# Kernel tuning notes

Hardware: AMD Instinct MI355X
Metric: run time of the kernel (lower is better)

## Reference

```python
import jax, jax.numpy as jnp
import numpy as np

B, T, L = 256, 512, 64


def setup_inputs() -> dict:
    key = jax.random.key(0)
    k1, k2, k3 = jax.random.split(key, 3)
    labels = jax.random.randint(k1, (B, T), 0, L)
    y_true = jax.nn.one_hot(labels, L, dtype=jnp.float32)  # [B,T,L] one-hot gold path
    y_pred = jax.random.normal(k2, (B, T, L), dtype=jnp.float32)  # emission scores
    # glorot_uniform init for trans [L,L]
    limit = np.sqrt(6.0 / (L + L)).astype(np.float32)
    trans = jax.random.uniform(k3, (L, L), dtype=jnp.float32, minval=-limit, maxval=limit)
    return {"y_true": y_true, "y_pred": y_pred, "trans": trans}


def reference(y_true, y_pred, trans):
    # ignore_last_label=False -> mask is None, all labels used.
    # Forward-algorithm log-partition via scan over time.
    init = y_pred[:, 0]  # [B,L]

    def step(state, emit_t):
        # state: [B,L] log-alpha; emit_t: [B,L]
        new = jax.nn.logsumexp(state[:, :, None] + trans[None, :, :], axis=1) + emit_t
        return new, None

    emits = jnp.swapaxes(y_pred[:, 1:], 0, 1)  # [T-1,B,L]
    last, _ = jax.lax.scan(step, init, emits)
    log_norm = jax.nn.logsumexp(last, axis=1, keepdims=True)  # [B,1]

    # path_score: per-label emission score + transition score along gold path
    point_score = jnp.sum(y_pred * y_true, axis=(1, 2))[:, None]  # [B,1]
    trans_score = jnp.einsum('bti,btj,ij->b', y_true[:, :-1], y_true[:, 1:], trans)[:, None]
    return -(point_score + trans_score - log_norm)  # [B,1] loss per example
```

## Files before the change

kernel.cpp:

```cpp
#include <hip/hip_runtime.h>
#include <hip/hip_bf16.h>
#include <cstdint>
#include <cstddef>


constexpr int Bc = 256, Tc = 512, Lc = 64;
#define LOG64F 4.1588830833596715f

typedef __attribute__((ext_vector_type(8))) short v8s;
typedef __attribute__((ext_vector_type(4))) float v4f;
typedef __attribute__((ext_vector_type(4))) unsigned int v4u;

__device__ __forceinline__ float lane_bcast(float v, int lane) {
    return __uint_as_float(__builtin_amdgcn_readlane(__float_as_uint(v), lane));
}
__device__ __forceinline__ int lane_bcast_i(int v, int lane) {
    return __builtin_amdgcn_readlane(v, lane);
}
__device__ __forceinline__ unsigned pk2(float x, float y) {
    const unsigned ux = __float_as_uint(x) + 0x8000u;
    const unsigned uy = __float_as_uint(y) + 0x8000u;
    return __builtin_amdgcn_perm(uy, ux, 0x07060302u);
}
__device__ __forceinline__ unsigned pk2t(float x, float y) {
    return __builtin_amdgcn_perm(__float_as_uint(y), __float_as_uint(x), 0x07060302u);
}
__device__ __forceinline__ v8s as_v8s(v4u u) {
    v8s r; __builtin_memcpy(&r, &u, 16); return r;
}
__device__ __forceinline__ unsigned short bf16b(float x) {
    return (unsigned short)((__float_as_uint(x) + 0x8000u) >> 16);
}

template<int CH>
__global__ __launch_bounds__(256, 2) void crf_pass1(
    const float* __restrict__ y_true,
    const float* __restrict__ y_pred,
    const float* __restrict__ trans,
    unsigned short* __restrict__ wsm,
    float* __restrict__ wss)
{
    constexpr int S = Tc / CH;
    const int tid = threadIdx.x, lane = tid & 63, wv = tid >> 6;
    const int w = blockIdx.x * 4 + wv;
    const int batch = w / CH;
    const int chunk = w % CH;
    const int q = lane >> 4, m16 = lane & 15;
    const int rsub = q, csub = m16;

    __shared__ alignas(16) unsigned char smem_raw[32768];
    float* strans = (float*)smem_raw;
    __shared__ alignas(16) float fbuf[4][4][Lc];

    {
        const v4f* t4 = (const v4f*)trans;
        #pragma unroll
        for (int k = 0; k < 4; ++k) {
            v4f v = t4[k * 256 + tid];
            *(v4f*)&strans[(k * 256 + tid) * 4] = v;
        }
    }
    __syncthreads();

    v8s Areg[4][2];
    #pragma unroll
    for (int I = 0; I < 4; ++I) {
        #pragma unroll
        for (int K = 0; K < 2; ++K) {
            float e[8];
            #pragma unroll
            for (int jj = 0; jj < 8; ++jj) {
                const int sig = (jj & 3) + 4 * q + 16 * (jj >> 2) + 32 * K;
                e[jj] = __expf(strans[sig * Lc + 16 * I + m16]);
            }
            v4u u;
            u.x = pk2(e[0], e[1]); u.y = pk2(e[2], e[3]);
            u.z = pk2(e[4], e[5]); u.w = pk2(e[6], e[7]);
            Areg[I][K] = as_v8s(u);
        }
    }

    const float* yp = y_pred + (size_t)batch * Tc * Lc;
    const float* yt = y_true + (size_t)batch * Tc * Lc;
    const v4f* yp4 = (const v4f*)yp;
    const v4f* yt4 = (const v4f*)yt;

    const int base = chunk * S;
    const int r0 = base + 1;
    float psum = 0.0f, tsum = 0.0f, c = 0.0f;
    int lbl_carry;
    {
        const float bt = yt[base * Lc + lane];
        lbl_carry = (int)__builtin_ctzll(__ballot(bt > 0.5f));
    }

    auto ld4 = [&](const v4f* p, int baseRow) -> v4f {
        int r = baseRow + rsub; r = (r < Tc - 1) ? r : (Tc - 1);
        return p[r * 16 + csub];
    };

    const v4f z4 = {0.f, 0.f, 0.f, 0.f};
    v4f cyp = ld4(yp4, r0), nyp = ld4(yp4, r0 + 4);
    v4f cyt = ld4(yt4, r0), nyt = ld4(yt4, r0 + 4);

    {
        const float k0 = lane_bcast(cyp.x, 0)  + LOG64F;
        const float k1 = lane_bcast(cyp.x, 16) + LOG64F;
        const float k2 = lane_bcast(cyp.x, 32) + LOG64F;
        const float k3 = lane_bcast(cyp.x, 48) + LOG64F;
        c += ((k0 + k1) + (k2 + k3));
        const float kk = (rsub & 1) ? ((rsub & 2) ? k3 : k1)
                                    : ((rsub & 2) ? k2 : k0);
        v4f f;
        f.x = __expf(cyp.x - kk); f.y = __expf(cyp.y - kk);
        f.z = __expf(cyp.z - kk); f.w = __expf(cyp.w - kk);
        *(v4f*)&fbuf[wv][rsub][4 * csub] = f;
    }

    v8s Bfr[2][4];
    #pragma unroll
    for (int Kc = 0; Kc < 2; ++Kc) {
        #pragma unroll
        for (int Jl = 0; Jl < 4; ++Jl) {
            v8s bb;
            #pragma unroll
            for (int jj = 0; jj < 8; ++jj) {
                const bool one = (m16 == 4 * q + (jj & 3)) &&
                                 (Jl == (jj >> 2) + 2 * Kc);
                bb[jj] = one ? (short)0x3F80 : (short)0;
            }
            Bfr[Kc][Jl] = bb;
        }
    }

    v4f P[4][4];
    #pragma unroll
    for (int I = 0; I < 4; ++I)
        #pragma unroll
        for (int Jl = 0; Jl < 4; ++Jl) P[I][Jl] = z4;

    auto mstep = [&](int s) {
        __builtin_amdgcn_s_setprio(1);
        #pragma unroll
        for (int I = 0; I < 4; ++I) {
            const v4f F = *(const v4f*)&fbuf[wv][s][16 * I + 4 * q];
            #pragma unroll
            for (int Jl = 0; Jl < 4; ++Jl) {
                v4f a = __builtin_amdgcn_mfma_f32_16x16x32_bf16(Areg[I][0], Bfr[0][Jl], z4, 0, 0, 0);
                a = __builtin_amdgcn_mfma_f32_16x16x32_bf16(Areg[I][1], Bfr[1][Jl], a, 0, 0, 0);
                P[I][Jl] = a * F;
            }
        }
        __builtin_amdgcn_s_setprio(0);
        #pragma unroll
        for (int Kc = 0; Kc < 2; ++Kc) {
            #pragma unroll
            for (int Jl = 0; Jl < 4; ++Jl) {
                v4u u;
                u.x = pk2t(P[2 * Kc][Jl].x,     P[2 * Kc][Jl].y);
                u.y = pk2t(P[2 * Kc][Jl].z,     P[2 * Kc][Jl].w);
                u.z = pk2t(P[2 * Kc + 1][Jl].x, P[2 * Kc + 1][Jl].y);
                u.w = pk2t(P[2 * Kc + 1][Jl].z, P[2 * Kc + 1][Jl].w);
                Bfr[Kc][Jl] = as_v8s(u);
            }
        }
    };

    auto scores4 = [&]() {
        psum = fmaf(cyp.x, cyt.x, psum); psum = fmaf(cyp.y, cyt.y, psum);
        psum = fmaf(cyp.z, cyt.z, psum); psum = fmaf(cyp.w, cyt.w, psum);
        const float has = fmaxf(fmaxf(cyt.x, cyt.y), fmaxf(cyt.z, cyt.w));
        int lidx = 0;
        lidx = (cyt.y > 0.5f) ? 1 : lidx;
        lidx = (cyt.z > 0.5f) ? 2 : lidx;
        lidx = (cyt.w > 0.5f) ? 3 : lidx;
        const unsigned long long m = __ballot(has > 0.5f);
        const int ln0 = (int)__builtin_ctz((unsigned)(m & 0xFFFFull));
        const int ln1 = (int)__builtin_ctz((unsigned)((m >> 16) & 0xFFFFull));
        const int ln2 = (int)__builtin_ctz((unsigned)((m >> 32) & 0xFFFFull));
        const int ln3 = (int)__builtin_ctz((unsigned)(m >> 48));
        const int lbl0 = 4 * ln0 + lane_bcast_i(lidx, ln0);
        const int lbl1 = 4 * ln1 + lane_bcast_i(lidx, 16 + ln1);
        const int lbl2 = 4 * ln2 + lane_bcast_i(lidx, 32 + ln2);
        const int lbl3 = 4 * ln3 + lane_bcast_i(lidx, 48 + ln3);
        const int lpA = (rsub & 2) ? lbl1 : lbl_carry;
        const int lpB = (rsub & 2) ? lbl2 : lbl0;
        const int lp  = (rsub & 1) ? lpB : lpA;
        lbl_carry = lbl3;
        const v4f tr = *(const v4f*)&strans[lp * Lc + 4 * csub];
        tsum = fmaf(cyt.x, tr.x, tsum); tsum = fmaf(cyt.y, tr.y, tsum);
        tsum = fmaf(cyt.z, tr.z, tsum); tsum = fmaf(cyt.w, tr.w, tsum);
    };

    #pragma unroll 1
    for (int bi = 0; bi < S / 4 - 1; ++bi) {
        const int rb = r0 + 4 * bi;
        const v4f lyp = ld4(yp4, rb + 8);
        const v4f lyt = ld4(yt4, rb + 8);

        scores4();
        mstep(0); mstep(1); mstep(2); mstep(3);

        {
            const float k0 = lane_bcast(nyp.x, 0)  + LOG64F;
            const float k1 = lane_bcast(nyp.x, 16) + LOG64F;
            const float k2 = lane_bcast(nyp.x, 32) + LOG64F;
            const float k3 = lane_bcast(nyp.x, 48) + LOG64F;
            c += ((k0 + k1) + k2);
            if (rb + 7 <= Tc - 1) c += k3;
            const float kk = (rsub & 1) ? ((rsub & 2) ? k3 : k1)
                                        : ((rsub & 2) ? k2 : k0);
            v4f f;
            f.x = __expf(nyp.x - kk); f.y = __expf(nyp.y - kk);
            f.z = __expf(nyp.z - kk); f.w = __expf(nyp.w - kk);
            *(v4f*)&fbuf[wv][rsub][4 * csub] = f;
        }
        cyp = nyp; nyp = lyp;
        cyt = nyt; nyt = lyt;
    }

    if (chunk < CH - 1) {
        scores4();
        mstep(0); mstep(1); mstep(2); mstep(3);
    } else {
        {
            float pd = cyp.x * cyt.x;
            pd = fmaf(cyp.y, cyt.y, pd); pd = fmaf(cyp.z, cyt.z, pd); pd = fmaf(cyp.w, cyt.w, pd);
            const float has = fmaxf(fmaxf(cyt.x, cyt.y), fmaxf(cyt.z, cyt.w));
            int lidx = 0;
            lidx = (cyt.y > 0.5f) ? 1 : lidx;
            lidx = (cyt.z > 0.5f) ? 2 : lidx;
            lidx = (cyt.w > 0.5f) ? 3 : lidx;
            const unsigned long long m = __ballot(has > 0.5f);
            const int ln0 = (int)__builtin_ctz((unsigned)(m & 0xFFFFull));
            const int ln1 = (int)__builtin_ctz((unsigned)((m >> 16) & 0xFFFFull));
            const int lbl0 = 4 * ln0 + lane_bcast_i(lidx, ln0);
            const int lbl1 = 4 * ln1 + lane_bcast_i(lidx, 16 + ln1);
            const int lpA = (rsub & 2) ? lbl1 : lbl_carry;
            const int lp  = (rsub & 1) ? lbl0 : lpA;
            const v4f tr = *(const v4f*)&strans[lp * Lc + 4 * csub];
            float td = cyt.x * tr.x;
            td = fmaf(cyt.y, tr.y, td); td = fmaf(cyt.z, tr.z, td); td = fmaf(cyt.w, tr.w, td);
            if (rsub < 3) { psum += pd; tsum += td; }
        }
        mstep(0); mstep(1); mstep(2);
    }

    __syncthreads();
    unsigned short* myblob = ((unsigned short*)smem_raw) + wv * 4096;
    #pragma unroll
    for (int I = 0; I < 4; ++I) {
        #pragma unroll
        for (int Jl = 0; Jl < 4; ++Jl) {
            float v[4] = {P[I][Jl].x, P[I][Jl].y, P[I][Jl].z, P[I][Jl].w};
            #pragma unroll
            for (int r = 0; r < 4; ++r) {
                const int row = 16 * (m16 >> 2) + 4 * q + r;
                const int gidx = I * 1024 + (Jl >> 1) * 512 + row * 8
                               + 4 * (Jl & 1) + (m16 & 3);
                myblob[gidx] = bf16b(v[r]);
            }
        }
    }
    {
        const unsigned short* src = myblob + lane * 64;
        unsigned short* dst = wsm + (size_t)(batch * CH + chunk) * 4096 + lane * 64;
        #pragma unroll
        for (int t = 0; t < 8; ++t)
            *(v4u*)(dst + t * 8) = *(const v4u*)(src + t * 8);
    }

    {
        #pragma unroll
        for (int k = 1; k < 64; k <<= 1) psum += __shfl_xor(psum, k);
        #pragma unroll
        for (int k = 1; k < 64; k <<= 1) tsum += __shfl_xor(tsum, k);
        if (lane == 0) {
            float* s = wss + (batch * CH + chunk) * 4;
            s[0] = c; s[1] = psum; s[2] = tsum;
        }
    }
}

template<int CH>
__global__ __launch_bounds__(64, 1) void crf_pass2(
    const float* __restrict__ y_true,
    const float* __restrict__ y_pred,
    const unsigned short* __restrict__ wsm,
    const float* __restrict__ wss,
    float* __restrict__ out)
{
    const int lane = threadIdx.x;
    const int b = blockIdx.x;
    const int q = lane >> 4;

    __shared__ float arow[Lc];

    const float* yp = y_pred + (size_t)b * Tc * Lc;
    const float yp0 = yp[lane];
    float psum = yp0 * (((const float*)(y_true + (size_t)b * Tc * Lc))[lane]);
    float tsum = 0.0f;
    float c = lane_bcast(yp0, 0);
    arow[lane] = __expf(yp0 - c);

    v8s Bfr[2];
    #pragma unroll
    for (int cc = 0; cc < 2; ++cc) {
        const v4f lo = *(const v4f*)&arow[32 * cc + 4 * q];
        const v4f hi = *(const v4f*)&arow[32 * cc + 16 + 4 * q];
        v4u u;
        u.x = pk2(lo.x, lo.y); u.y = pk2(lo.z, lo.w);
        u.z = pk2(hi.x, hi.y); u.w = pk2(hi.z, hi.w);
        Bfr[cc] = as_v8s(u);
    }

    const v4f z4 = {0.f, 0.f, 0.f, 0.f};
    v4f P0 = z4, P1 = z4, P2 = z4, P3 = z4;

    v4u Abuf[2][8];
    {
        const v4u* g0 = (const v4u*)(wsm + (size_t)(b * CH) * 4096);
        #pragma unroll
        for (int s = 0; s < 8; ++s) Abuf[0][s] = g0[s * 64 + lane];
    }

    #pragma unroll
    for (int kk = 0; kk < CH; ++kk) {
        const int cur = kk & 1, nxt = cur ^ 1;
        if (kk < CH - 1) {
            const v4u* g1 = (const v4u*)(wsm + (size_t)(b * CH + kk + 1) * 4096);
            #pragma unroll
            for (int s = 0; s < 8; ++s) Abuf[nxt][s] = g1[s * 64 + lane];
        }
        v4f a0 = __builtin_amdgcn_mfma_f32_16x16x32_bf16(as_v8s(Abuf[cur][0]), Bfr[0], z4, 0, 0, 0);
        v4f a1 = __builtin_amdgcn_mfma_f32_16x16x32_bf16(as_v8s(Abuf[cur][2]), Bfr[0], z4, 0, 0, 0);
        v4f a2 = __builtin_amdgcn_mfma_f32_16x16x32_bf16(as_v8s(Abuf[cur][4]), Bfr[0], z4, 0, 0, 0);
        v4f a3 = __builtin_amdgcn_mfma_f32_16x16x32_bf16(as_v8s(Abuf[cur][6]), Bfr[0], z4, 0, 0, 0);
        a0 = __builtin_amdgcn_mfma_f32_16x16x32_bf16(as_v8s(Abuf[cur][1]), Bfr[1], a0, 0, 0, 0);
        a1 = __builtin_amdgcn_mfma_f32_16x16x32_bf16(as_v8s(Abuf[cur][3]), Bfr[1], a1, 0, 0, 0);
        a2 = __builtin_amdgcn_mfma_f32_16x16x32_bf16(as_v8s(Abuf[cur][5]), Bfr[1], a2, 0, 0, 0);
        a3 = __builtin_amdgcn_mfma_f32_16x16x32_bf16(as_v8s(Abuf[cur][7]), Bfr[1], a3, 0, 0, 0);

        const float sc = lane_bcast(a0.x, 0);
        const float inv = 1.0f / sc;
        c += __logf(sc);
        P0 = a0 * inv; P1 = a1 * inv; P2 = a2 * inv; P3 = a3 * inv;
        {
            v4u u;
            u.x = pk2(P0.x, P0.y); u.y = pk2(P0.z, P0.w);
            u.z = pk2(P1.x, P1.y); u.w = pk2(P1.z, P1.w);
            Bfr[0] = as_v8s(u);
        }
        {
            v4u u;
            u.x = pk2(P2.x, P2.y); u.y = pk2(P2.z, P2.w);
            u.z = pk2(P3.x, P3.y); u.w = pk2(P3.z, P3.w);
            Bfr[1] = as_v8s(u);
        }
    }

    float ftot = (((P0.x + P0.y) + (P0.z + P0.w)) + ((P1.x + P1.y) + (P1.z + P1.w)))
               + (((P2.x + P2.y) + (P2.z + P2.w)) + ((P3.x + P3.y) + (P3.z + P3.w)));
    ftot += __shfl_xor(ftot, 16);
    ftot += __shfl_xor(ftot, 32);

    #pragma unroll
    for (int k = 1; k < 64; k <<= 1) psum += __shfl_xor(psum, k);

    if (lane == 0) {
        float cs = c, ps = psum, ts = tsum;
        #pragma unroll
        for (int kk = 0; kk < CH; ++kk) {
            const float* s = wss + (b * CH + kk) * 4;
            cs += s[0]; ps += s[1]; ts += s[2];
        }
        out[b] = -(ps + ts - (cs + __logf(ftot)));
    }
}

extern "C" void kernel_launch(void* const* d_in, const int* in_sizes, int n_in,
                              void* d_out, int out_size, void* d_ws, size_t ws_size,
                              hipStream_t stream) {
    const float* y_true = (const float*)d_in[0];
    const float* y_pred = (const float*)d_in[1];
    const float* trans  = (const float*)d_in[2];
    float* outp = (float*)d_out;
    unsigned short* wsm = (unsigned short*)d_ws;

    float* wss = (float*)((char*)d_ws + (16ull << 20));
    crf_pass1<8><<<dim3(512), dim3(256), 0, stream>>>(y_true, y_pred, trans, wsm, wss);
    crf_pass2<8><<<dim3(256),  dim3(64),  0, stream>>>(y_true, y_pred, wsm, wss, outp);
}
```

Before: 147.0 us.

## Switch chunk transfer-matrix products from 16x16x32 to 32x32x16 bf16 MFMA tiles

Reorganizes the per-step 64x64 transfer-matrix multiply to use 2x2 tiles of 32x32x16 bf16 MFMA instead of 4x4 tiles of 16x16x32. The A/B register fragments, the scaling by emission factors, the repacking of the result into the next B operand, and the final blob write-out layout are all remapped to the 32x32 output layout. The goal is fewer MFMA issues per step and possibly higher MFMA throughput on the serial dependency chain. The trade-off is longer dependent accumulation chains of four MFMAs each and a different register footprint.

```diff
diff --git a/kernel.cpp b/kernel.cpp
--- a/kernel.cpp
+++ b/kernel.cpp
@@ -9,6 +9,7 @@
 
 typedef __attribute__((ext_vector_type(8))) short v8s;
 typedef __attribute__((ext_vector_type(4))) float v4f;
+typedef __attribute__((ext_vector_type(16))) float v16f;
 typedef __attribute__((ext_vector_type(4))) unsigned int v4u;
 
 __device__ __forceinline__ float lane_bcast(float v, int lane) {
@@ -47,6 +48,7 @@
     const int chunk = w % CH;
     const int q = lane >> 4, m16 = lane & 15;
     const int rsub = q, csub = m16;
+    const int lo5 = lane & 31, lhi = lane >> 5;
 
     __shared__ alignas(16) unsigned char smem_raw[32768];
     float* strans = (float*)smem_raw;
@@ -62,21 +64,22 @@
     }
     __syncthreads();
 
-    v8s Areg[4][2];
-    #pragma unroll
-    for (int I = 0; I < 4; ++I) {
-        #pragma unroll
-        for (int K = 0; K < 2; ++K) {
+    v8s Areg[2][4];
+    #pragma unroll
+    for (int ti = 0; ti < 2; ++ti) {
+        #pragma unroll
+        for (int kc = 0; kc < 4; ++kc) {
             float e[8];
             #pragma unroll
             for (int jj = 0; jj < 8; ++jj) {
-                const int sig = (jj & 3) + 4 * q + 16 * (jj >> 2) + 32 * K;
-                e[jj] = __expf(strans[sig * Lc + 16 * I + m16]);
+                const int from = 16 * kc + (jj & 3) + 4 * lhi + 8 * (jj >> 2);
+                const int to   = 32 * ti + lo5;
+                e[jj] = __expf(strans[from * Lc + to]);
             }
             v4u u;
             u.x = pk2(e[0], e[1]); u.y = pk2(e[2], e[3]);
             u.z = pk2(e[4], e[5]); u.w = pk2(e[6], e[7]);
-            Areg[I][K] = as_v8s(u);
+            Areg[ti][kc] = as_v8s(u);
         }
     }
 
@@ -117,51 +120,66 @@
         *(v4f*)&fbuf[wv][rsub][4 * csub] = f;
     }
 
-    v8s Bfr[2][4];
-    #pragma unroll
-    for (int Kc = 0; Kc < 2; ++Kc) {
-        #pragma unroll
-        for (int Jl = 0; Jl < 4; ++Jl) {
+    v8s Bfr[4][2];
+    #pragma unroll
+    for (int kc = 0; kc < 4; ++kc) {
+        #pragma unroll
+        for (int tj = 0; tj < 2; ++tj) {
             v8s bb;
             #pragma unroll
             for (int jj = 0; jj < 8; ++jj) {
-                const bool one = (m16 == 4 * q + (jj & 3)) &&
-                                 (Jl == (jj >> 2) + 2 * Kc);
-                bb[jj] = one ? (short)0x3F80 : (short)0;
+                const int kg = 16 * kc + (jj & 3) + 4 * lhi + 8 * (jj >> 2);
+                const int ng = 32 * tj + lo5;
+                bb[jj] = (kg == ng) ? (short)0x3F80 : (short)0;
             }
-            Bfr[Kc][Jl] = bb;
-        }
-    }
-
-    v4f P[4][4];
-    #pragma unroll
-    for (int I = 0; I < 4; ++I)
-        #pragma unroll
-        for (int Jl = 0; Jl < 4; ++Jl) P[I][Jl] = z4;
+            Bfr[kc][tj] = bb;
+        }
+    }
+
+    v16f P[2][2];
+    #pragma unroll
+    for (int ti = 0; ti < 2; ++ti)
+        #pragma unroll
+        for (int tj = 0; tj < 2; ++tj)
+            #pragma unroll
+            for (int r = 0; r < 16; ++r) P[ti][tj][r] = 0.f;
+
+    const v16f z16 = P[0][0];
 
     auto mstep = [&](int s) {
         __builtin_amdgcn_s_setprio(1);
         #pragma unroll
-        for (int I = 0; I < 4; ++I) {
-            const v4f F = *(const v4f*)&fbuf[wv][s][16 * I + 4 * q];
-            #pragma unroll
-            for (int Jl = 0; Jl < 4; ++Jl) {
-                v4f a = __builtin_amdgcn_mfma_f32_16x16x32_bf16(Areg[I][0], Bfr[0][Jl], z4, 0, 0, 0);
-                a = __builtin_amdgcn_mfma_f32_16x16x32_bf16(Areg[I][1], Bfr[1][Jl], a, 0, 0, 0);
-                P[I][Jl] = a * F;
+        for (int ti = 0; ti < 2; ++ti) {
+            v4f Fv[4];
+            #pragma unroll
+            for (int rq = 0; rq < 4; ++rq)
+                Fv[rq] = *(const v4f*)&fbuf[wv][s][32 * ti + 8 * rq + 4 * lhi];
+            #pragma unroll
+            for (int tj = 0; tj < 2; ++tj) {
+                v16f a = __builtin_amdgcn_mfma_f32_32x32x16_bf16(Areg[ti][0], Bfr[0][tj], z16, 0, 0, 0);
+                a = __builtin_amdgcn_mfma_f32_32x32x16_bf16(Areg[ti][1], Bfr[1][tj], a, 0, 0, 0);
+                a = __builtin_amdgcn_mfma_f32_32x32x16_bf16(Areg[ti][2], Bfr[2][tj], a, 0, 0, 0);
+                a = __builtin_amdgcn_mfma_f32_32x32x16_bf16(Areg[ti][3], Bfr[3][tj], a, 0, 0, 0);
+                #pragma unroll
+                for (int r = 0; r < 16; ++r)
+                    a[r] = a[r] * Fv[r >> 2][r & 3];
+                P[ti][tj] = a;
             }
         }
         __builtin_amdgcn_s_setprio(0);
         #pragma unroll
-        for (int Kc = 0; Kc < 2; ++Kc) {
-            #pragma unroll
-            for (int Jl = 0; Jl < 4; ++Jl) {
-                v4u u;
-                u.x = pk2t(P[2 * Kc][Jl].x,     P[2 * Kc][Jl].y);
-                u.y = pk2t(P[2 * Kc][Jl].z,     P[2 * Kc][Jl].w);
-                u.z = pk2t(P[2 * Kc + 1][Jl].x, P[2 * Kc + 1][Jl].y);
-                u.w = pk2t(P[2 * Kc + 1][Jl].z, P[2 * Kc + 1][Jl].w);
-                Bfr[Kc][Jl] = as_v8s(u);
+        for (int ti = 0; ti < 2; ++ti) {
+            #pragma unroll
+            for (int tj = 0; tj < 2; ++tj) {
+                #pragma unroll
+                for (int b = 0; b < 2; ++b) {
+                    v4u u;
+                    u.x = pk2t(P[ti][tj][8 * b + 0], P[ti][tj][8 * b + 1]);
+                    u.y = pk2t(P[ti][tj][8 * b + 2], P[ti][tj][8 * b + 3]);
+                    u.z = pk2t(P[ti][tj][8 * b + 4], P[ti][tj][8 * b + 5]);
+                    u.w = pk2t(P[ti][tj][8 * b + 6], P[ti][tj][8 * b + 7]);
+                    Bfr[2 * ti + b][tj] = as_v8s(u);
+                }
             }
         }
     };
@@ -249,16 +267,17 @@
     __syncthreads();
     unsigned short* myblob = ((unsigned short*)smem_raw) + wv * 4096;
     #pragma unroll
-    for (int I = 0; I < 4; ++I) {
-        #pragma unroll
-        for (int Jl = 0; Jl < 4; ++Jl) {
-            float v[4] = {P[I][Jl].x, P[I][Jl].y, P[I][Jl].z, P[I][Jl].w};
-            #pragma unroll
-            for (int r = 0; r < 4; ++r) {
-                const int row = 16 * (m16 >> 2) + 4 * q + r;
-                const int gidx = I * 1024 + (Jl >> 1) * 512 + row * 8
-                               + 4 * (Jl & 1) + (m16 & 3);
-                myblob[gidx] = bf16b(v[r]);
+    for (int ti = 0; ti < 2; ++ti) {
+        #pragma unroll
+        for (int tj = 0; tj < 2; ++tj) {
+            #pragma unroll
+            for (int r = 0; r < 16; ++r) {
+                const int to = 32 * ti + (r & 3) + 8 * (r >> 2) + 4 * lhi;
+                const int fr = 32 * tj + lo5;
+                const int li = (to >> 4) * 1024 + (fr >> 5) * 512
+                             + (16 * ((fr & 15) >> 2) + (to & 15)) * 8
+                             + 4 * ((fr >> 4) & 1) + (fr & 3);
+                myblob[li] = bf16b(P[ti][tj][r]);
             }
         }
     }
```

Result: faster. 143.6 us (-2.3%).

## Interleave two independent time chunks per wavefront to hide MFMA dependency latency

Applied to the files above, without the earlier changes.

Each wavefront now processes two time chunks of the same batch instead of one, alternating the matrix-product steps of the two independent chains. The aim is to hide the serial MFMA→pack→MFMA dependency latency of one chain behind the other's work. The pass-1 grid is halved to match. This doubles register use for accumulators and B fragments, which could cause spills or lower occupancy, and it halves the number of waves available to the scheduler.

```diff
diff --git a/kernel.cpp b/kernel.cpp
--- a/kernel.cpp
+++ b/kernel.cpp
@@ -43,14 +43,14 @@
     constexpr int S = Tc / CH;
     const int tid = threadIdx.x, lane = tid & 63, wv = tid >> 6;
     const int w = blockIdx.x * 4 + wv;
-    const int batch = w / CH;
-    const int chunk = w % CH;
+    const int batch = w >> 2;
+    const int c0 = 2 * (w & 3), c1 = c0 + 1;
     const int q = lane >> 4, m16 = lane & 15;
     const int rsub = q, csub = m16;
 
     __shared__ alignas(16) unsigned char smem_raw[32768];
     float* strans = (float*)smem_raw;
-    __shared__ alignas(16) float fbuf[4][4][Lc];
+    __shared__ alignas(16) float fbuf[4][2][4][Lc];
 
     {
         const v4f* t4 = (const v4f*)trans;
@@ -85,13 +85,17 @@
     const v4f* yp4 = (const v4f*)yp;
     const v4f* yt4 = (const v4f*)yt;
 
-    const int base = chunk * S;
-    const int r0 = base + 1;
-    float psum = 0.0f, tsum = 0.0f, c = 0.0f;
-    int lbl_carry;
+    const int r0A = c0 * S + 1, r0B = c1 * S + 1;
+    float psA = 0.f, tsA = 0.f, cA = 0.f;
+    float psB = 0.f, tsB = 0.f, cB = 0.f;
+    int lblA, lblB;
     {
-        const float bt = yt[base * Lc + lane];
-        lbl_carry = (int)__builtin_ctzll(__ballot(bt > 0.5f));
+        const float bt = yt[c0 * S * Lc + lane];
+        lblA = (int)__builtin_ctzll(__ballot(bt > 0.5f));
+    }
+    {
+        const float bt = yt[c1 * S * Lc + lane];
+        lblB = (int)__builtin_ctzll(__ballot(bt > 0.5f));
     }
 
     auto ld4 = [&](const v4f* p, int baseRow) -> v4f {
@@ -100,10 +104,12 @@
     };
 
     const v4f z4 = {0.f, 0.f, 0.f, 0.f};
-    v4f cyp = ld4(yp4, r0), nyp = ld4(yp4, r0 + 4);
-    v4f cyt = ld4(yt4, r0), nyt = ld4(yt4, r0 + 4);
-
-    {
+    v4f cypA = ld4(yp4, r0A), nypA = ld4(yp4, r0A + 4);
+    v4f cytA = ld4(yt4, r0A), nytA = ld4(yt4, r0A + 4);
+    v4f cypB = ld4(yp4, r0B), nypB = ld4(yp4, r0B + 4);
+    v4f cytB = ld4(yt4, r0B), nytB = ld4(yt4, r0B + 4);
+
+    auto prolF = [&](const v4f& cyp, int csel, float& c) {
         const float k0 = lane_bcast(cyp.x, 0)  + LOG64F;
         const float k1 = lane_bcast(cyp.x, 16) + LOG64F;
         const float k2 = lane_bcast(cyp.x, 32) + LOG64F;
@@ -114,10 +120,27 @@
         v4f f;
         f.x = __expf(cyp.x - kk); f.y = __expf(cyp.y - kk);
         f.z = __expf(cyp.z - kk); f.w = __expf(cyp.w - kk);
-        *(v4f*)&fbuf[wv][rsub][4 * csub] = f;
-    }
-
-    v8s Bfr[2][4];
+        *(v4f*)&fbuf[wv][csel][rsub][4 * csub] = f;
+    };
+    prolF(cypA, 0, cA);
+    prolF(cypB, 1, cB);
+
+    auto postF = [&](const v4f& nyp, int csel, float& c, int rb) {
+        const float k0 = lane_bcast(nyp.x, 0)  + LOG64F;
+        const float k1 = lane_bcast(nyp.x, 16) + LOG64F;
+        const float k2 = lane_bcast(nyp.x, 32) + LOG64F;
+        const float k3 = lane_bcast(nyp.x, 48) + LOG64F;
+        c += ((k0 + k1) + k2);
+        if (rb + 7 <= Tc - 1) c += k3;
+        const float kk = (rsub & 1) ? ((rsub & 2) ? k3 : k1)
+                                    : ((rsub & 2) ? k2 : k0);
+        v4f f;
+        f.x = __expf(nyp.x - kk); f.y = __expf(nyp.y - kk);
+        f.z = __expf(nyp.z - kk); f.w = __expf(nyp.w - kk);
+        *(v4f*)&fbuf[wv][csel][rsub][4 * csub] = f;
+    };
+
+    v8s BfrA[2][4], BfrB[2][4];
     #pragma unroll
     for (int Kc = 0; Kc < 2; ++Kc) {
         #pragma unroll
@@ -129,21 +152,22 @@
                                  (Jl == (jj >> 2) + 2 * Kc);
                 bb[jj] = one ? (short)0x3F80 : (short)0;
             }
-            Bfr[Kc][Jl] = bb;
-        }
-    }
-
-    v4f P[4][4];
+            BfrA[Kc][Jl] = bb;
+            BfrB[Kc][Jl] = bb;
+        }
+    }
+
+    v4f PA[4][4], PB[4][4];
     #pragma unroll
     for (int I = 0; I < 4; ++I)
         #pragma unroll
-        for (int Jl = 0; Jl < 4; ++Jl) P[I][Jl] = z4;
-
-    auto mstep = [&](int s) {
+        for (int Jl = 0; Jl < 4; ++Jl) { PA[I][Jl] = z4; PB[I][Jl] = z4; }
+
+    auto mstep = [&](int s, int csel, v8s (&Bfr)[2][4], v4f (&P)[4][4]) {
         __builtin_amdgcn_s_setprio(1);
         #pragma unroll
         for (int I = 0; I < 4; ++I) {
-            const v4f F = *(const v4f*)&fbuf[wv][s][16 * I + 4 * q];
+            const v4f F = *(const v4f*)&fbuf[wv][csel][s][16 * I + 4 * q];
             #pragma unroll
             for (int Jl = 0; Jl < 4; ++Jl) {
                 v4f a = __builtin_amdgcn_mfma_f32_16x16x32_bf16(Areg[I][0], Bfr[0][Jl], z4, 0, 0, 0);
@@ -166,7 +190,8 @@
         }
     };
 
-    auto scores4 = [&]() {
+    auto scores4 = [&](const v4f& cyp, const v4f& cyt, int& lbl_carry,
+                       float& psum, float& tsum) {
         psum = fmaf(cyp.x, cyt.x, psum); psum = fmaf(cyp.y, cyt.y, psum);
         psum = fmaf(cyp.z, cyt.z, psum); psum = fmaf(cyp.w, cyt.w, psum);
         const float has = fmaxf(fmaxf(cyt.x, cyt.y), fmaxf(cyt.z, cyt.w));
@@ -194,90 +219,100 @@
 
     #pragma unroll 1
     for (int bi = 0; bi < S / 4 - 1; ++bi) {
-        const int rb = r0 + 4 * bi;
-        const v4f lyp = ld4(yp4, rb + 8);
-        const v4f lyt = ld4(yt4, rb + 8);
-
-        scores4();
-        mstep(0); mstep(1); mstep(2); mstep(3);
-
-        {
-            const float k0 = lane_bcast(nyp.x, 0)  + LOG64F;
-            const float k1 = lane_bcast(nyp.x, 16) + LOG64F;
-            const float k2 = lane_bcast(nyp.x, 32) + LOG64F;
-            const float k3 = lane_bcast(nyp.x, 48) + LOG64F;
-            c += ((k0 + k1) + k2);
-            if (rb + 7 <= Tc - 1) c += k3;
-            const float kk = (rsub & 1) ? ((rsub & 2) ? k3 : k1)
-                                        : ((rsub & 2) ? k2 : k0);
-            v4f f;
-            f.x = __expf(nyp.x - kk); f.y = __expf(nyp.y - kk);
-            f.z = __expf(nyp.z - kk); f.w = __expf(nyp.w - kk);
-            *(v4f*)&fbuf[wv][rsub][4 * csub] = f;
-        }
-        cyp = nyp; nyp = lyp;
-        cyt = nyt; nyt = lyt;
-    }
-
-    if (chunk < CH - 1) {
-        scores4();
-        mstep(0); mstep(1); mstep(2); mstep(3);
+        const int rbA = r0A + 4 * bi;
+        const int rbB = r0B + 4 * bi;
+        const v4f lypA = ld4(yp4, rbA + 8);
+        const v4f lytA = ld4(yt4, rbA + 8);
+        const v4f lypB = ld4(yp4, rbB + 8);
+        const v4f lytB = ld4(yt4, rbB + 8);
+
+        scores4(cypA, cytA, lblA, psA, tsA);
+        scores4(cypB, cytB, lblB, psB, tsB);
+
+        mstep(0, 0, BfrA, PA); mstep(0, 1, BfrB, PB);
+        mstep(1, 0, BfrA, PA); mstep(1, 1, BfrB, PB);
+        mstep(2, 0, BfrA, PA); mstep(2, 1, BfrB, PB);
+        mstep(3, 0, BfrA, PA); mstep(3, 1, BfrB, PB);
+
+        postF(nypA, 0, cA, rbA);
+        postF(nypB, 1, cB, rbB);
+
+        cypA = nypA; nypA = lypA; cytA = nytA; nytA = lytA;
+        cypB = nypB; nypB = lypB; cytB = nytB; nytB = lytB;
+    }
+
+    const bool tailB = (c1 == CH - 1);
+    scores4(cypA, cytA, lblA, psA, tsA);
+    if (!tailB) {
+        scores4(cypB, cytB, lblB, psB, tsB);
     } else {
-        {
-            float pd = cyp.x * cyt.x;
-            pd = fmaf(cyp.y, cyt.y, pd); pd = fmaf(cyp.z, cyt.z, pd); pd = fmaf(cyp.w, cyt.w, pd);
-            const float has = fmaxf(fmaxf(cyt.x, cyt.y), fmaxf(cyt.z, cyt.w));
-            int lidx = 0;
-            lidx = (cyt.y > 0.5f) ? 1 : lidx;
-            lidx = (cyt.z > 0.5f) ? 2 : lidx;
-            lidx = (cyt.w > 0.5f) ? 3 : lidx;
-            const unsigned long long m = __ballot(has > 0.5f);
-            const int ln0 = (int)__builtin_ctz((unsigned)(m & 0xFFFFull));
-            const int ln1 = (int)__builtin_ctz((unsigned)((m >> 16) & 0xFFFFull));
-            const int lbl0 = 4 * ln0 + lane_bcast_i(lidx, ln0);
-            const int lbl1 = 4 * ln1 + lane_bcast_i(lidx, 16 + ln1);
-            const int lpA = (rsub & 2) ? lbl1 : lbl_carry;
-            const int lp  = (rsub & 1) ? lbl0 : lpA;
-            const v4f tr = *(const v4f*)&strans[lp * Lc + 4 * csub];
-            float td = cyt.x * tr.x;
-            td = fmaf(cyt.y, tr.y, td); td = fmaf(cyt.z, tr.z, td); td = fmaf(cyt.w, tr.w, td);
-            if (rsub < 3) { psum += pd; tsum += td; }
-        }
-        mstep(0); mstep(1); mstep(2);
-    }
+        float pd = cypB.x * cytB.x;
+        pd = fmaf(cypB.y, cytB.y, pd); pd = fmaf(cypB.z, cytB.z, pd); pd = fmaf(cypB.w, cytB.w, pd);
+        const float has = fmaxf(fmaxf(cytB.x, cytB.y), fmaxf(cytB.z, cytB.w));
+        int lidx = 0;
+        lidx = (cytB.y > 0.5f) ? 1 : lidx;
+        lidx = (cytB.z > 0.5f) ? 2 : lidx;
+        lidx = (cytB.w > 0.5f) ? 3 : lidx;
+        const unsigned long long m = __ballot(has > 0.5f);
+        const int ln0 = (int)__builtin_ctz((unsigned)(m & 0xFFFFull));
+        const int ln1 = (int)__builtin_ctz((unsigned)((m >> 16) & 0xFFFFull));
+        const int lbl0 = 4 * ln0 + lane_bcast_i(lidx, ln0);
+        const int lbl1 = 4 * ln1 + lane_bcast_i(lidx, 16 + ln1);
+        const int lpA_ = (rsub & 2) ? lbl1 : lblB;
+        const int lp  = (rsub & 1) ? lbl0 : lpA_;
+        const v4f tr = *(const v4f*)&strans[lp * Lc + 4 * csub];
+        float td = cytB.x * tr.x;
+        td = fmaf(cytB.y, tr.y, td); td = fmaf(cytB.z, tr.z, td); td = fmaf(cytB.w, tr.w, td);
+        if (rsub < 3) { psB += pd; tsB += td; }
+    }
+
+    mstep(0, 0, BfrA, PA); mstep(0, 1, BfrB, PB);
+    mstep(1, 0, BfrA, PA); mstep(1, 1, BfrB, PB);
+    mstep(2, 0, BfrA, PA); mstep(2, 1, BfrB, PB);
+    mstep(3, 0, BfrA, PA);
+    if (!tailB) mstep(3, 1, BfrB, PB);
 
     __syncthreads();
     unsigned short* myblob = ((unsigned short*)smem_raw) + wv * 4096;
-    #pragma unroll
-    for (int I = 0; I < 4; ++I) {
-        #pragma unroll
-        for (int Jl = 0; Jl < 4; ++Jl) {
-            float v[4] = {P[I][Jl].x, P[I][Jl].y, P[I][Jl].z, P[I][Jl].w};
-            #pragma unroll
-            for (int r = 0; r < 4; ++r) {
-                const int row = 16 * (m16 >> 2) + 4 * q + r;
-                const int gidx = I * 1024 + (Jl >> 1) * 512 + row * 8
-                               + 4 * (Jl & 1) + (m16 & 3);
-                myblob[gidx] = bf16b(v[r]);
+
+    auto scatter_out = [&](v4f (&P)[4][4], int chunk) {
+        #pragma unroll
+        for (int I = 0; I < 4; ++I) {
+            #pragma unroll
+            for (int Jl = 0; Jl < 4; ++Jl) {
+                float v[4] = {P[I][Jl].x, P[I][Jl].y, P[I][Jl].z, P[I][Jl].w};
+                #pragma unroll
+                for (int r = 0; r < 4; ++r) {
+                    const int row = 16 * (m16 >> 2) + 4 * q + r;
+                    const int gidx = I * 1024 + (Jl >> 1) * 512 + row * 8
+                                   + 4 * (Jl & 1) + (m16 & 3);
+                    myblob[gidx] = bf16b(v[r]);
+                }
             }
         }
-    }
-    {
         const unsigned short* src = myblob + lane * 64;
         unsigned short* dst = wsm + (size_t)(batch * CH + chunk) * 4096 + lane * 64;
         #pragma unroll
         for (int t = 0; t < 8; ++t)
             *(v4u*)(dst + t * 8) = *(const v4u*)(src + t * 8);
-    }
+    };
+    scatter_out(PA, c0);
+    scatter_out(PB, c1);
 
     {
         #pragma unroll
-        for (int k = 1; k < 64; k <<= 1) psum += __shfl_xor(psum, k);
-        #pragma unroll
-        for (int k = 1; k < 64; k <<= 1) tsum += __shfl_xor(tsum, k);
+        for (int k = 1; k < 64; k <<= 1) psA += __shfl_xor(psA, k);
+        #pragma unroll
+        for (int k = 1; k < 64; k <<= 1) tsA += __shfl_xor(tsA, k);
+        #pragma unroll
+        for (int k = 1; k < 64; k <<= 1) psB += __shfl_xor(psB, k);
+        #pragma unroll
+        for (int k = 1; k < 64; k <<= 1) tsB += __shfl_xor(tsB, k);
         if (lane == 0) {
-            float* s = wss + (batch * CH + chunk) * 4;
-            s[0] = c; s[1] = psum; s[2] = tsum;
+            float* sA = wss + (batch * CH + c0) * 4;
+            sA[0] = cA; sA[1] = psA; sA[2] = tsA;
+            float* sB = wss + (batch * CH + c1) * 4;
+            sB[0] = cB; sB[1] = psB; sB[2] = tsB;
         }
     }
 }
@@ -388,6 +423,6 @@
     unsigned short* wsm = (unsigned short*)d_ws;
 
     float* wss = (float*)((char*)d_ws + (16ull << 20));
-    crf_pass1<8><<<dim3(512), dim3(256), 0, stream>>>(y_true, y_pred, trans, wsm, wss);
-    crf_pass2<8><<<dim3(256),  dim3(64),  0, stream>>>(y_true, y_pred, wsm, wss, outp);
-}
+    crf_pass1<8><<<dim3(256), dim3(256), 0, stream>>>(y_true, y_pred, trans, wsm, wss);
+    crf_pass2<8><<<dim3(256), dim3(64),  0, stream>>>(y_true, y_pred, wsm, wss, outp);
+}
```

After: 155.8 us. 1.06x slower.
